# Kernel tuning notes

Hardware: AMD Instinct MI355X
Metric: run time of the kernel (lower is better)

## Reference

```python
import jax, jax.numpy as jnp
import numpy as np

B, S, H, NH = 1, 2048, 4096, 32
HD = H // NH
INV_NORM = 1.0 / np.sqrt(HD)


def _alibi_slopes(n_heads):
    # standard Bloom ALiBi slopes
    closest_pow2 = 2 ** int(np.floor(np.log2(n_heads)))
    base = 2.0 ** (-(2.0 ** -(np.log2(closest_pow2) - 3)))
    slopes = base ** np.arange(1, closest_pow2 + 1)
    if closest_pow2 != n_heads:
        extra_base = 2.0 ** (-(2.0 ** -(np.log2(2 * closest_pow2) - 3)))
        extra = extra_base ** np.arange(1, 2 * (n_heads - closest_pow2) + 1, 2)
        slopes = np.concatenate([slopes, extra])
    return slopes.astype(np.float32)


def setup_inputs() -> dict:
    key = jax.random.key(0)
    ks = jax.random.split(key, 6)
    hidden_states = jax.random.normal(ks[0], (B, S, H), dtype=jnp.float32)
    residual = jax.random.normal(ks[1], (B, S, H), dtype=jnp.float32)
    # ALiBi bias: slopes[h] * position, shape [B*NH, 1, S]
    slopes = jnp.asarray(_alibi_slopes(NH))  # [NH]
    pos = jnp.arange(S, dtype=jnp.float32)  # [S]
    alibi = (slopes[:, None] * pos[None, :])[:, None, :]  # [NH,1,S]
    alibi = jnp.tile(alibi, (B, 1, 1))  # [B*NH,1,S]
    # causal mask: True = masked out
    attention_mask = ~jnp.tril(jnp.ones((S, S), dtype=bool))[None, None]  # [1,1,S,S]
    qkv_w = jax.random.normal(ks[2], (3 * H, H), dtype=jnp.float32) * 0.02
    qkv_b = jax.random.normal(ks[3], (3 * H,), dtype=jnp.float32) * 0.02
    dense_w = jax.random.normal(ks[4], (H, H), dtype=jnp.float32) * 0.02
    dense_b = jax.random.normal(ks[5], (H,), dtype=jnp.float32) * 0.02
    return {
        "hidden_states": hidden_states,
        "residual": residual,
        "alibi": alibi,
        "attention_mask": attention_mask,
        "qkv_w": qkv_w,
        "qkv_b": qkv_b,
        "dense_w": dense_w,
        "dense_b": dense_b,
    }


def reference(hidden_states, residual, alibi, attention_mask, qkv_w, qkv_b, dense_w, dense_b):
    b, s, h = hidden_states.shape
    fused = hidden_states @ qkv_w.T + qkv_b  # [B,S,3H]
    fused = fused.reshape(b, s, NH, 3, HD)  # per-head interleaved q,k,v
    q, k, v = fused[..., 0, :], fused[..., 1, :], fused[..., 2, :]  # [B,S,NH,HD]
    # scores = beta*alibi + inv_norm * q @ k^T
    scores = jnp.einsum("bqnd,bknd->bnqk", q, k) * INV_NORM
    scores = scores + alibi.reshape(b, NH, 1, s)  # broadcast over q
    scores = jnp.where(attention_mask, jnp.finfo(scores.dtype).min, scores)
    probs = jax.nn.softmax(scores.astype(jnp.float32), axis=-1)  # [B,NH,S,S]
    ctx = jnp.einsum("bnqk,bknd->bqnd", probs, v).reshape(b, s, h)
    out = ctx @ dense_w.T + dense_b
    return residual + out  # dropout_add with p=0 / eval mode
```

## Files before the change

### kernel.cpp

```cpp
#include <hip/hip_runtime.h>
#include <cstdint>
#include <cstddef>

typedef unsigned short u16;
typedef __attribute__((ext_vector_type(8))) __bf16 bf16x8;
typedef __attribute__((ext_vector_type(4))) float f32x4;

#define S_LEN   2048
#define H_DIM   4096
#define NH_N    32
#define HD_N    128
#define QKV_LD  12288

__device__ __forceinline__ u16 f2b(float f) {
  union { float f; unsigned u; } v; v.f = f;
  unsigned r = v.u + 0x7fffu + ((v.u >> 16) & 1u);
  return (u16)(r >> 16);
}

__device__ __forceinline__ void gl2lds16(const void* g, void* l) {
  __builtin_amdgcn_global_load_lds((__attribute__((address_space(1))) void*)g,
                                   (__attribute__((address_space(3))) void*)l,
                                   16, 0, 0);
}

__global__ __launch_bounds__(256) void cvt_kernel(const float* __restrict__ src,
                                                  u16* __restrict__ dst, int n8) {
  int i = blockIdx.x * 256 + threadIdx.x;
  if (i >= n8) return;
  const float4* s4 = (const float4*)src;
  float4 a = s4[i * 2], b = s4[i * 2 + 1];
  union { u16 o[8]; uint4 v; } u;
  u.o[0] = f2b(a.x); u.o[1] = f2b(a.y); u.o[2] = f2b(a.z); u.o[3] = f2b(a.w);
  u.o[4] = f2b(b.x); u.o[5] = f2b(b.y); u.o[6] = f2b(b.z); u.o[7] = f2b(b.w);
  ((uint4*)dst)[i] = u.v;
}

template <int OUTF32>
__global__ __launch_bounds__(256, 2)
void gemm_kernel(const u16* __restrict__ A, const u16* __restrict__ B,
                 const float* __restrict__ bias, const float* __restrict__ resid,
                 u16* __restrict__ outB, float* __restrict__ outF,
                 int M, int N, int K) {
  __shared__ __align__(16) u16 As[128 * 64];
  __shared__ __align__(16) u16 Bs[128 * 64];
  const int tid  = threadIdx.x;
  const int lane = tid & 63;
  const int wave = tid >> 6;
  const int l15  = lane & 15;
  const int quad = lane >> 4;
  const int m0 = blockIdx.y * 128;
  const int n0 = blockIdx.x * 128;
  const int wm = (wave & 1) * 64;
  const int wn = (wave >> 1) * 64;

  f32x4 acc[4][4] = {};

  int sRow[4], sCol[4];
#pragma unroll
  for (int it = 0; it < 4; ++it) {
    int slot = wave * 256 + it * 64 + lane;
    int row  = slot >> 3;
    int kc   = (slot & 7) ^ (row & 7);
    sRow[it] = row;
    sCol[it] = kc * 8;
  }
  const u16* Ag = A + (size_t)m0 * K;
  const u16* Bg = B + (size_t)n0 * K;

  for (int kb = 0; kb < K; kb += 64) {
#pragma unroll
    for (int it = 0; it < 4; ++it) {
      int base = (wave * 256 + it * 64) * 8;
      gl2lds16(Ag + (size_t)sRow[it] * K + kb + sCol[it], &As[base]);
      gl2lds16(Bg + (size_t)sRow[it] * K + kb + sCol[it], &Bs[base]);
    }
    __syncthreads();
#pragma unroll
    for (int s = 0; s < 2; ++s) {
      const int kc = s * 4 + quad;
      bf16x8 af[4], bfr[4];
#pragma unroll
      for (int i = 0; i < 4; ++i) {
        int ra = wm + i * 16 + l15;
        af[i]  = *(const bf16x8*)&As[(ra * 8 + (kc ^ (ra & 7))) * 8];
        int rb = wn + i * 16 + l15;
        bfr[i] = *(const bf16x8*)&Bs[(rb * 8 + (kc ^ (rb & 7))) * 8];
      }
#pragma unroll
      for (int i = 0; i < 4; ++i)
#pragma unroll
        for (int j = 0; j < 4; ++j)
          acc[i][j] = __builtin_amdgcn_mfma_f32_16x16x32_bf16(af[i], bfr[j], acc[i][j], 0, 0, 0);
    }
    __syncthreads();
  }

  float bcol[4];
#pragma unroll
  for (int j = 0; j < 4; ++j) bcol[j] = bias[n0 + wn + j * 16 + l15];
#pragma unroll
  for (int i = 0; i < 4; ++i) {
    int rowb = m0 + wm + i * 16 + quad * 4;
#pragma unroll
    for (int r = 0; r < 4; ++r) {
      size_t rowoff = (size_t)(rowb + r) * N;
#pragma unroll
      for (int j = 0; j < 4; ++j) {
        int col = n0 + wn + j * 16 + l15;
        float v = acc[i][j][r] + bcol[j];
        if (OUTF32) outF[rowoff + col] = v + resid[rowoff + col];
        else        outB[rowoff + col] = f2b(v);
      }
    }
  }
}

__global__ __launch_bounds__(256, 2)
void attn_kernel(const u16* __restrict__ QKV, const float* __restrict__ alibi,
                 u16* __restrict__ CTX) {
  __shared__ __align__(16) u16 Ks[64 * 128];
  __shared__ __align__(16) u16 Vt[128 * 64];
  __shared__ __align__(16) u16 Ps[4 * 1024];
  const int tid  = threadIdx.x;
  const int lane = tid & 63;
  const int wave = tid >> 6;
  const int l15  = lane & 15;
  const int quad = lane >> 4;
  const int qt   = (int)gridDim.x - 1 - (int)blockIdx.x;
  const int head = blockIdx.y;
  const int q0   = qt * 64;
  const int qcol = head * 384;
  const int kcol = qcol + 128;
  const int vcol = qcol + 256;
  const float c1 = 0.08838834764831845f * 1.4426950408889634f;
  const float slope2 = alibi[head * S_LEN + 1] * 1.4426950408889634f;

  bf16x8 qf[4];
  {
    const u16* qp = QKV + (size_t)(q0 + wave * 16 + l15) * QKV_LD + qcol;
#pragma unroll
    for (int s = 0; s < 4; ++s) qf[s] = *(const bf16x8*)(qp + s * 32 + quad * 8);
  }

  float m_i[4], l_i[4];
#pragma unroll
  for (int r = 0; r < 4; ++r) { m_i[r] = -3.0e38f; l_i[r] = 0.0f; }
  f32x4 acc[8] = {};

  const int nk = qt + 1;
  for (int kt = 0; kt < nk; ++kt) {
    const int k0 = kt * 64;
#pragma unroll
    for (int it = 0; it < 4; ++it) {
      int slot = wave * 256 + it * 64 + lane;
      int row  = slot >> 4;
      int hdc  = (slot & 15) ^ (row & 15);
      gl2lds16(QKV + (size_t)(k0 + row) * QKV_LD + kcol + hdc * 8,
               &Ks[(wave * 256 + it * 64) * 8]);
    }
#pragma unroll
    for (int it = 0; it < 4; ++it) {
      int c   = it * 256 + tid;
      int key = c & 63;
      int hd0 = (c >> 6) * 8;
      const u16* vp = QKV + (size_t)(k0 + key) * QKV_LD + vcol + hd0;
      union { uint4 v; u16 e[8]; } t; t.v = *(const uint4*)vp;
#pragma unroll
      for (int uu = 0; uu < 8; ++uu) {
        int hd = hd0 + uu;
        Vt[(hd * 8 + ((key >> 3) ^ (hd & 7))) * 8 + (key & 7)] = t.e[uu];
      }
    }
    __syncthreads();

    f32x4 sc[4] = {};
#pragma unroll
    for (int s = 0; s < 4; ++s) {
      const int kc = s * 4 + quad;
      bf16x8 kf[4];
#pragma unroll
      for (int j = 0; j < 4; ++j) {
        int row = j * 16 + l15;
        kf[j] = *(const bf16x8*)&Ks[(row * 16 + (kc ^ (row & 15))) * 8];
      }
#pragma unroll
      for (int j = 0; j < 4; ++j)
        sc[j] = __builtin_amdgcn_mfma_f32_16x16x32_bf16(qf[s], kf[j], sc[j], 0, 0, 0);
    }

    const bool diag = (kt == qt);
    float xv[4][4];
    float mt[4] = { -3.0e38f, -3.0e38f, -3.0e38f, -3.0e38f };
#pragma unroll
    for (int j = 0; j < 4; ++j) {
      int key  = k0 + j * 16 + l15;
      float al = slope2 * (float)key;
#pragma unroll
      for (int r = 0; r < 4; ++r) {
        float x = sc[j][r] * c1 + al;
        if (diag) {
          int qrow = q0 + wave * 16 + quad * 4 + r;
          if (key > qrow) x = -3.0e38f;
        }
        xv[j][r] = x;
        mt[r] = fmaxf(mt[r], x);
      }
    }
#pragma unroll
    for (int r = 0; r < 4; ++r) {
      float v = mt[r];
      v = fmaxf(v, __shfl_xor(v, 1));
      v = fmaxf(v, __shfl_xor(v, 2));
      v = fmaxf(v, __shfl_xor(v, 4));
      v = fmaxf(v, __shfl_xor(v, 8));
      mt[r] = fmaxf(m_i[r], v);
    }
    float alpha[4], psum[4];
#pragma unroll
    for (int r = 0; r < 4; ++r) {
      alpha[r] = exp2f(m_i[r] - mt[r]);
      m_i[r] = mt[r];
      psum[r] = 0.0f;
    }
#pragma unroll
    for (int j = 0; j < 4; ++j) {
      int col = j * 16 + l15;
      int kc  = col >> 3;
#pragma unroll
      for (int r = 0; r < 4; ++r) {
        float p = exp2f(xv[j][r] - m_i[r]);
        psum[r] += p;
        int qrow = quad * 4 + r;
        Ps[wave * 1024 + (qrow * 8 + (kc ^ (qrow & 7))) * 8 + (col & 7)] = f2b(p);
      }
    }
#pragma unroll
    for (int r = 0; r < 4; ++r) {
      float v = psum[r];
      v += __shfl_xor(v, 1);
      v += __shfl_xor(v, 2);
      v += __shfl_xor(v, 4);
      v += __shfl_xor(v, 8);
      l_i[r] = l_i[r] * alpha[r] + v;
    }
#pragma unroll
    for (int t = 0; t < 8; ++t)
#pragma unroll
      for (int r = 0; r < 4; ++r) acc[t][r] *= alpha[r];

#pragma unroll
    for (int s = 0; s < 2; ++s) {
      const int kc = s * 4 + quad;
      bf16x8 pf = *(const bf16x8*)&Ps[wave * 1024 + (l15 * 8 + (kc ^ (l15 & 7))) * 8];
#pragma unroll
      for (int t = 0; t < 8; ++t) {
        int row = t * 16 + l15;
        bf16x8 vf = *(const bf16x8*)&Vt[(row * 8 + (kc ^ (row & 7))) * 8];
        acc[t] = __builtin_amdgcn_mfma_f32_16x16x32_bf16(pf, vf, acc[t], 0, 0, 0);
      }
    }
    __syncthreads();
  }

#pragma unroll
  for (int r = 0; r < 4; ++r) {
    float inv = 1.0f / l_i[r];
    size_t rowoff = (size_t)(q0 + wave * 16 + quad * 4 + r) * H_DIM;
#pragma unroll
    for (int t = 0; t < 8; ++t)
      CTX[rowoff + head * HD_N + t * 16 + l15] = f2b(acc[t][r] * inv);
  }
}

extern "C" void kernel_launch(void* const* d_in, const int* in_sizes, int n_in,
                              void* d_out, int out_size, void* d_ws, size_t ws_size,
                              hipStream_t stream) {
  const float* hidden   = (const float*)d_in[0];
  const float* residual = (const float*)d_in[1];
  const float* alibi    = (const float*)d_in[2];
  const float* qkv_w    = (const float*)d_in[4];
  const float* qkv_b    = (const float*)d_in[5];
  const float* dense_w  = (const float*)d_in[6];
  const float* dense_b  = (const float*)d_in[7];
  float* out = (float*)d_out;

  u16* Xb  = (u16*)d_ws;
  u16* Wq  = Xb + (size_t)S_LEN * H_DIM;
  u16* Wd  = Wq + (size_t)3 * H_DIM * H_DIM;
  u16* QKV = Wd + (size_t)H_DIM * H_DIM;
  u16* CTX = QKV + (size_t)S_LEN * 3 * H_DIM;

  {
    int n8 = S_LEN * H_DIM / 8;
    cvt_kernel<<<dim3((n8 + 255) / 256), 256, 0, stream>>>(hidden, Xb, n8);
  }
  {
    int n8 = 3 * H_DIM * H_DIM / 8;
    cvt_kernel<<<dim3((n8 + 255) / 256), 256, 0, stream>>>(qkv_w, Wq, n8);
  }
  {
    int n8 = H_DIM * H_DIM / 8;
    cvt_kernel<<<dim3((n8 + 255) / 256), 256, 0, stream>>>(dense_w, Wd, n8);
  }

  gemm_kernel<0><<<dim3(3 * H_DIM / 128, S_LEN / 128), 256, 0, stream>>>(
      Xb, Wq, qkv_b, nullptr, QKV, nullptr, S_LEN, 3 * H_DIM, H_DIM);

  attn_kernel<<<dim3(S_LEN / 64, NH_N), 256, 0, stream>>>(QKV, alibi, CTX);

  gemm_kernel<1><<<dim3(H_DIM / 128, S_LEN / 128), 256, 0, stream>>>(
      CTX, Wd, dense_b, residual, nullptr, out, S_LEN, H_DIM, H_DIM);
}
```

Measured before the change: 860.1 us.

## Write V transposed from QKV GEMM and double-buffer K/V tiles in attention

The QKV GEMM epilogue now writes Q and K into a compact per-head buffer and V pre-transposed per head (head, dim, seq). The attention kernel then loads both K and V tiles with direct global-to-LDS copies instead of scalar-scattered V transposes, and double-buffers them so the next tile's loads overlap the current tile's compute. LDS usage rises to two K and two V buffers, which may lower occupancy. The V epilogue writes are 8-byte strided stores across the sequence dimension.

```diff
diff --git a/kernel.cpp b/kernel.cpp
--- a/kernel.cpp
+++ b/kernel.cpp
@@ -10,7 +10,7 @@
 #define H_DIM   4096
 #define NH_N    32
 #define HD_N    128
-#define QKV_LD  12288
+#define QK_LD   8192
 
 __device__ __forceinline__ u16 f2b(float f) {
   union { float f; unsigned u; } v; v.f = f;
@@ -40,7 +40,8 @@
 __global__ __launch_bounds__(256, 2)
 void gemm_kernel(const u16* __restrict__ A, const u16* __restrict__ B,
                  const float* __restrict__ bias, const float* __restrict__ resid,
-                 u16* __restrict__ outB, float* __restrict__ outF,
+                 u16* __restrict__ outQK, u16* __restrict__ outVT,
+                 float* __restrict__ outF,
                  int M, int N, int K) {
   __shared__ __align__(16) u16 As[128 * 64];
   __shared__ __align__(16) u16 Bs[128 * 64];
@@ -96,31 +97,45 @@
     __syncthreads();
   }
 
-  float bcol[4];
-#pragma unroll
-  for (int j = 0; j < 4; ++j) bcol[j] = bias[n0 + wn + j * 16 + l15];
 #pragma unroll
   for (int i = 0; i < 4; ++i) {
     int rowb = m0 + wm + i * 16 + quad * 4;
 #pragma unroll
-    for (int r = 0; r < 4; ++r) {
-      size_t rowoff = (size_t)(rowb + r) * N;
-#pragma unroll
-      for (int j = 0; j < 4; ++j) {
-        int col = n0 + wn + j * 16 + l15;
-        float v = acc[i][j][r] + bcol[j];
-        if (OUTF32) outF[rowoff + col] = v + resid[rowoff + col];
-        else        outB[rowoff + col] = f2b(v);
+    for (int j = 0; j < 4; ++j) {
+      int c0 = n0 + wn + j * 16;
+      float bb = bias[c0 + l15];
+      if (OUTF32) {
+#pragma unroll
+        for (int r = 0; r < 4; ++r) {
+          size_t rowoff = (size_t)(rowb + r) * N;
+          outF[rowoff + c0 + l15] = acc[i][j][r] + bb + resid[rowoff + c0 + l15];
+        }
+      } else {
+        int head = c0 / 384;
+        int rem  = c0 % 384;
+        int part = rem >> 7;
+        if (part == 2) {
+          int d = (rem & 127) + l15;
+          union { ushort4 v; u16 e[4]; } pk;
+#pragma unroll
+          for (int r = 0; r < 4; ++r) pk.e[r] = f2b(acc[i][j][r] + bb);
+          *(ushort4*)&outVT[(size_t)head * (HD_N * S_LEN) + (size_t)d * S_LEN + rowb] = pk.v;
+        } else {
+          int colq = head * 256 + part * 128 + (rem & 127) + l15;
+#pragma unroll
+          for (int r = 0; r < 4; ++r)
+            outQK[(size_t)(rowb + r) * QK_LD + colq] = f2b(acc[i][j][r] + bb);
+        }
       }
     }
   }
 }
 
 __global__ __launch_bounds__(256, 2)
-void attn_kernel(const u16* __restrict__ QKV, const float* __restrict__ alibi,
-                 u16* __restrict__ CTX) {
-  __shared__ __align__(16) u16 Ks[64 * 128];
-  __shared__ __align__(16) u16 Vt[128 * 64];
+void attn_kernel(const u16* __restrict__ QK, const u16* __restrict__ VT,
+                 const float* __restrict__ alibi, u16* __restrict__ CTX) {
+  __shared__ __align__(16) u16 Ks[2][64 * 128];
+  __shared__ __align__(16) u16 Vs[2][128 * 64];
   __shared__ __align__(16) u16 Ps[4 * 1024];
   const int tid  = threadIdx.x;
   const int lane = tid & 63;
@@ -130,15 +145,27 @@
   const int qt   = (int)gridDim.x - 1 - (int)blockIdx.x;
   const int head = blockIdx.y;
   const int q0   = qt * 64;
-  const int qcol = head * 384;
-  const int kcol = qcol + 128;
-  const int vcol = qcol + 256;
   const float c1 = 0.08838834764831845f * 1.4426950408889634f;
   const float slope2 = alibi[head * S_LEN + 1] * 1.4426950408889634f;
 
+  const u16* Kbase = QK + head * 256 + 128;
+  const u16* Vbase = VT + (size_t)head * (HD_N * S_LEN);
+
+  int kRow[4], kCol[4], vRow[4], vCol[4];
+#pragma unroll
+  for (int it = 0; it < 4; ++it) {
+    int slot = wave * 256 + it * 64 + lane;
+    int kr = slot >> 4;
+    kRow[it] = kr;
+    kCol[it] = ((slot & 15) ^ (kr & 15)) * 8;
+    int d = slot >> 3;
+    vRow[it] = d;
+    vCol[it] = ((slot & 7) ^ (d & 7)) * 8;
+  }
+
   bf16x8 qf[4];
   {
-    const u16* qp = QKV + (size_t)(q0 + wave * 16 + l15) * QKV_LD + qcol;
+    const u16* qp = QK + (size_t)(q0 + wave * 16 + l15) * QK_LD + head * 256;
 #pragma unroll
     for (int s = 0; s < 4; ++s) qf[s] = *(const bf16x8*)(qp + s * 32 + quad * 8);
   }
@@ -149,30 +176,27 @@
   f32x4 acc[8] = {};
 
   const int nk = qt + 1;
+
+#pragma unroll
+  for (int it = 0; it < 4; ++it) {
+    int base = (wave * 256 + it * 64) * 8;
+    gl2lds16(Kbase + (size_t)kRow[it] * QK_LD + kCol[it], &Ks[0][base]);
+    gl2lds16(Vbase + (size_t)vRow[it] * S_LEN + vCol[it], &Vs[0][base]);
+  }
+  __syncthreads();
+
+  int cur = 0;
   for (int kt = 0; kt < nk; ++kt) {
     const int k0 = kt * 64;
-#pragma unroll
-    for (int it = 0; it < 4; ++it) {
-      int slot = wave * 256 + it * 64 + lane;
-      int row  = slot >> 4;
-      int hdc  = (slot & 15) ^ (row & 15);
-      gl2lds16(QKV + (size_t)(k0 + row) * QKV_LD + kcol + hdc * 8,
-               &Ks[(wave * 256 + it * 64) * 8]);
-    }
-#pragma unroll
-    for (int it = 0; it < 4; ++it) {
-      int c   = it * 256 + tid;
-      int key = c & 63;
-      int hd0 = (c >> 6) * 8;
-      const u16* vp = QKV + (size_t)(k0 + key) * QKV_LD + vcol + hd0;
-      union { uint4 v; u16 e[8]; } t; t.v = *(const uint4*)vp;
-#pragma unroll
-      for (int uu = 0; uu < 8; ++uu) {
-        int hd = hd0 + uu;
-        Vt[(hd * 8 + ((key >> 3) ^ (hd & 7))) * 8 + (key & 7)] = t.e[uu];
-      }
-    }
-    __syncthreads();
+    if (kt + 1 < nk) {
+      const int kn = k0 + 64;
+#pragma unroll
+      for (int it = 0; it < 4; ++it) {
+        int base = (wave * 256 + it * 64) * 8;
+        gl2lds16(Kbase + (size_t)(kn + kRow[it]) * QK_LD + kCol[it], &Ks[cur ^ 1][base]);
+        gl2lds16(Vbase + (size_t)vRow[it] * S_LEN + kn + vCol[it], &Vs[cur ^ 1][base]);
+      }
+    }
 
     f32x4 sc[4] = {};
 #pragma unroll
@@ -182,7 +206,7 @@
 #pragma unroll
       for (int j = 0; j < 4; ++j) {
         int row = j * 16 + l15;
-        kf[j] = *(const bf16x8*)&Ks[(row * 16 + (kc ^ (row & 15))) * 8];
+        kf[j] = *(const bf16x8*)&Ks[cur][(row * 16 + (kc ^ (row & 15))) * 8];
       }
 #pragma unroll
       for (int j = 0; j < 4; ++j)
@@ -256,11 +280,12 @@
 #pragma unroll
       for (int t = 0; t < 8; ++t) {
         int row = t * 16 + l15;
-        bf16x8 vf = *(const bf16x8*)&Vt[(row * 8 + (kc ^ (row & 7))) * 8];
+        bf16x8 vf = *(const bf16x8*)&Vs[cur][(row * 8 + (kc ^ (row & 7))) * 8];
         acc[t] = __builtin_amdgcn_mfma_f32_16x16x32_bf16(pf, vf, acc[t], 0, 0, 0);
       }
     }
     __syncthreads();
+    cur ^= 1;
   }
 
 #pragma unroll
@@ -288,8 +313,9 @@
   u16* Xb  = (u16*)d_ws;
   u16* Wq  = Xb + (size_t)S_LEN * H_DIM;
   u16* Wd  = Wq + (size_t)3 * H_DIM * H_DIM;
-  u16* QKV = Wd + (size_t)H_DIM * H_DIM;
-  u16* CTX = QKV + (size_t)S_LEN * 3 * H_DIM;
+  u16* QKb = Wd + (size_t)H_DIM * H_DIM;
+  u16* VT  = QKb + (size_t)S_LEN * QK_LD;
+  u16* CTX = VT + (size_t)NH_N * HD_N * S_LEN;
 
   {
     int n8 = S_LEN * H_DIM / 8;
@@ -305,10 +331,10 @@
   }
 
   gemm_kernel<0><<<dim3(3 * H_DIM / 128, S_LEN / 128), 256, 0, stream>>>(
-      Xb, Wq, qkv_b, nullptr, QKV, nullptr, S_LEN, 3 * H_DIM, H_DIM);
-
-  attn_kernel<<<dim3(S_LEN / 64, NH_N), 256, 0, stream>>>(QKV, alibi, CTX);
+      Xb, Wq, qkv_b, nullptr, QKb, VT, nullptr, S_LEN, 3 * H_DIM, H_DIM);
+
+  attn_kernel<<<dim3(S_LEN / 64, NH_N), 256, 0, stream>>>(QKb, VT, alibi, CTX);
 
   gemm_kernel<1><<<dim3(H_DIM / 128, S_LEN / 128), 256, 0, stream>>>(
-      CTX, Wd, dense_b, residual, nullptr, out, S_LEN, H_DIM, H_DIM);
-}
+      CTX, Wd, dense_b, residual, nullptr, nullptr, out, S_LEN, H_DIM, H_DIM);
+}
```

Result: faster. 835.0 us (-2.9%).
